# Kernel optimization log

Measured on AMD Instinct MI355X. Metric: run time of the kernel, lower is better.

Reference implementation:

```python
import jax, jax.numpy as jnp
import numpy as np
from jax import lax

TAU = 2.0        # LIF membrane time constant
EPS = 1e-5       # BatchNorm eps
ALPHA = 4.0      # surrogate sigmoid sharpness (spikingjelly default)
HEADS = 8
SCALE = 0.125

@jax.custom_vjp
def heaviside(x):
    return (x >= 0.0).astype(x.dtype)

def _h_fwd(x):
    return heaviside(x), x

def _h_bwd(x, g):
    s = jax.nn.sigmoid(ALPHA * x)
    return (g * ALPHA * s * (1.0 - s),)

heaviside.defvjp(_h_fwd, _h_bwd)

def lif(x, vth):
    # multi-step LIF over leading time axis; hard reset to 0, detach_reset=True
    def step(v, xt):
        v = v + (xt - v) / TAU
        s = heaviside(v - vth)
        v = v * (1.0 - lax.stop_gradient(s))
        return v, s
    _, spikes = lax.scan(step, jnp.zeros_like(x[0]), x)
    return spikes

def conv_bn(x, W, gamma, beta, b=None):
    # 1x1 Conv1d == channel GEMM; BN in training mode (batch stats over (TB, N))
    y = jnp.einsum('oc,tcn->ton', W, x)
    if b is not None:
        y = y + b[None, :, None]
    mu = y.mean(axis=(0, 2), keepdims=True)
    var = y.var(axis=(0, 2), keepdims=True)
    return gamma[None, :, None] * (y - mu) * lax.rsqrt(var + EPS) + beta[None, :, None]

def setup_inputs() -> dict:
    key = jax.random.key(0)
    ks = jax.random.split(key, 8)
    T, B, C, H, W = 4, 16, 512, 16, 16
    s = 1.0 / np.sqrt(C)
    return {
        'x': jax.random.normal(ks[0], (T, B, C, H, W), dtype=jnp.float32),
        'qW': jax.random.normal(ks[1], (C, C), dtype=jnp.float32) * s,
        'q_gamma': jnp.ones((C,), jnp.float32), 'q_beta': jnp.zeros((C,), jnp.float32),
        'kW': jax.random.normal(ks[2], (C, C), dtype=jnp.float32) * s,
        'k_gamma': jnp.ones((C,), jnp.float32), 'k_beta': jnp.zeros((C,), jnp.float32),
        'vW': jax.random.normal(ks[3], (C, C), dtype=jnp.float32) * s,
        'v_gamma': jnp.ones((C,), jnp.float32), 'v_beta': jnp.zeros((C,), jnp.float32),
        'projW': jax.random.normal(ks[4], (C, C), dtype=jnp.float32) * s,
        'proj_b': jnp.zeros((C,), jnp.float32),
        'proj_gamma': jnp.ones((C,), jnp.float32), 'proj_beta': jnp.zeros((C,), jnp.float32),
    }

def reference(x, qW, q_gamma, q_beta, kW, k_gamma, k_beta, vW, v_gamma, v_beta,
              projW, proj_b, proj_gamma, proj_beta):
    T, B, C, H, W = x.shape
    N = H * W
    d = C // HEADS
    xf = x.reshape(T * B, C, N)

    def branch(Wc, g, b):
        y = conv_bn(xf, Wc, g, b).reshape(T, B, C, N)
        s = lif(y, 1.0)                               # binary spikes [T,B,C,N]
        # -> [T,B,heads,N,d]
        return s.transpose(0, 1, 3, 2).reshape(T, B, N, HEADS, d).transpose(0, 1, 3, 2, 4)

    q = branch(qW, q_gamma, q_beta)
    k = branch(kW, k_gamma, k_beta)
    v = branch(vW, v_gamma, v_beta)

    kv = jnp.einsum('tbhnd,tbhne->tbhde', k, v)       # linear attention [d,d]
    a = jnp.einsum('tbhnd,tbhde->tbhne', q, kv) * SCALE
    a = a.transpose(0, 1, 2, 4, 3).reshape(T, B, C, N)
    a = lif(a, 0.5).reshape(T * B, C, N)              # attn_lif, vth=0.5

    out = conv_bn(a, projW, proj_gamma, proj_beta, proj_b).reshape(T, B, C, N)
    out = lif(out, 1.0)
    return out.reshape(T, B, C, W, H)
```

## Files before the change

### kernel.cpp

```cpp
#include <hip/hip_runtime.h>

#define T_ 4
#define B_ 16
#define C_ 512
#define N_ 256
#define TB_ 64

using u64 = unsigned long long;
typedef int v4i __attribute__((ext_vector_type(4)));


__device__ __forceinline__ void digitize6(float xf, double scale, int d[6]) {
  double m = (double)xf * scale;
  long long t = (long long)rint(m);
#pragma unroll
  for (int s = 5; s >= 0; --s) {
    int dig = (int)((t + 128) & 255) - 128;
    d[s] = dig;
    t = (t - dig) >> 8;
  }
}

__device__ __forceinline__ void digitize5(float xf, double scale, int d[5]) {
  double m = (double)xf * scale;
  long long t = (long long)rint(m);
#pragma unroll
  for (int s = 4; s >= 0; --s) {
    int dig = (int)((t + 128) & 255) - 128;
    d[s] = dig;
    t = (t - dig) >> 8;
  }
}

__device__ __forceinline__ void dig4(float xv, int d[4]) {
  float c = fminf(fmaxf(xv, -7.999999f), 7.999999f);
  int m = (int)rintf(c * 268435456.0f);
#pragma unroll
  for (int t = 3; t >= 0; --t) {
    int dd = ((m + 128) & 255) - 128;
    d[t] = dd;
    m = (m - dd) >> 8;
  }
}

__device__ __forceinline__ void gload16(const void* g, void* l) {
  __builtin_amdgcn_global_load_lds(
      (const __attribute__((address_space(1))) unsigned int*)(unsigned long long)g,
      (__attribute__((address_space(3))) unsigned int*)(unsigned long long)l,
      16, 0, 0);
}


__global__ __launch_bounds__(256) void predig_x(
    const float* __restrict__ X, char* __restrict__ Xd4)
{
  const int cb = blockIdx.x * 64;
  const int nb = blockIdx.y * 64;
  const int tb = blockIdx.z;
  const int n  = threadIdx.x & 63;
  const int c0 = (threadIdx.x >> 6) * 16;
  int dg[16][4];
#pragma unroll
  for (int j = 0; j < 16; ++j) {
    float xv = X[((size_t)tb * C_ + cb + c0 + j) * N_ + nb + n];
    dig4(xv, dg[j]);
  }
#pragma unroll
  for (int t = 0; t < 4; ++t) {
    unsigned w[4];
#pragma unroll
    for (int q = 0; q < 4; ++q)
      w[q] = (unsigned)(dg[4*q+0][t] & 255)
           | ((unsigned)(dg[4*q+1][t] & 255) << 8)
           | ((unsigned)(dg[4*q+2][t] & 255) << 16)
           | ((unsigned)(dg[4*q+3][t] & 255) << 24);
    uint4 u; u.x = w[0]; u.y = w[1]; u.z = w[2]; u.w = w[3];
    *reinterpret_cast<uint4*>(
        &Xd4[(((size_t)tb * N_ + nb + n) * 4 + t) * C_ + cb + c0]) = u;
  }
}

__global__ __launch_bounds__(128) void decomp_w5i(
    const float* __restrict__ W, char* __restrict__ Wsl)
{
  const int o = blockIdx.x;
  const int k4 = threadIdx.x * 4;
  float4 w4 = *reinterpret_cast<const float4*>(&W[(size_t)o * C_ + k4]);
  int d[4][5];
  digitize5(w4.x, 0x1p39, d[0]);
  digitize5(w4.y, 0x1p39, d[1]);
  digitize5(w4.z, 0x1p39, d[2]);
  digitize5(w4.w, 0x1p39, d[3]);
#pragma unroll
  for (int s = 0; s < 5; ++s) {
    unsigned u = (unsigned)(d[0][s] & 255) | ((unsigned)(d[1][s] & 255) << 8)
               | ((unsigned)(d[2][s] & 255) << 16) | ((unsigned)(d[3][s] & 255) << 24);
    *reinterpret_cast<unsigned*>(&Wsl[((size_t)o * 5 + s) * C_ + k4]) = u;
  }
}

template<int XP>
__global__ __launch_bounds__(256) void gemm_s(
    const char* __restrict__ Bp, const char* __restrict__ Wsl,
    double* __restrict__ Y)
{
  __shared__ v4i Als[2][5][64][4];
  __shared__ v4i Bls[2][XP][64][4];
  const int tb = blockIdx.z;
  const int ob = blockIdx.y * 64;
  const int nb = blockIdx.x * 64;
  const int tid = threadIdx.x;
  const int lane = tid & 63;
  const int wv = tid >> 6;
  const int wo = wv * 16;
  const int lr = lane & 15;
  const int lg = lane >> 4;

  v4i acc[5][4] = {};

  const int sow = wv * 16 + (lane >> 2);
  const int acs = (lane & 3) ^ ((sow >> 1) & 3);
  const char* asrc[5];
#pragma unroll
  for (int s = 0; s < 5; ++s)
    asrc[s] = Wsl + ((size_t)(ob + sow) * 5 + s) * C_ + acs * 16;

  const int s_slot = lane & 3;
  const char* bsrc[(XP == 4) ? 4 : 1];
  if (XP == 4) {
#pragma unroll
    for (int r = 0; r < 4; ++r) {
      int sn = r * 16 + (lane >> 2);
      bsrc[r] = Bp + (((size_t)tb * N_ + nb + sn) * 4 + wv) * C_
              + ((s_slot ^ ((sn >> 1) & 3)) * 16);
    }
  } else {
    int sn = wv * 16 + (lane >> 2);
    bsrc[0] = Bp + ((size_t)tb * N_ + nb + sn) * C_
            + ((s_slot ^ ((sn >> 1) & 3)) * 16);
  }

#define STAGE_(buf, cb) do {                                              \
    _Pragma("unroll")                                                     \
    for (int s_ = 0; s_ < 5; ++s_)                                        \
      gload16(asrc[s_] + (cb), &Als[buf][s_][wv * 16][0]);                \
    if (XP == 4) {                                                        \
      _Pragma("unroll")                                                   \
      for (int r_ = 0; r_ < 4; ++r_)                                      \
        gload16(bsrc[r_] + (cb), &Bls[buf][wv][r_ * 16][0]);              \
    } else {                                                              \
      gload16(bsrc[0] + (cb), &Bls[buf][0][wv * 16][0]);                  \
    }                                                                     \
  } while (0)

  STAGE_(0, 0);
  __syncthreads();

#pragma unroll
  for (int i = 0; i < 8; ++i) {
    const int cur = i & 1;
    const int cb = i * 64;
    if (i < 7) STAGE_(cur ^ 1, cb + 64);
    __builtin_amdgcn_sched_barrier(0);
    v4i Af[5];
#pragma unroll
    for (int s = 0; s < 5; ++s) {
      const int o = wo + lr;
      Af[s] = Als[cur][s][o][lg ^ ((o >> 1) & 3)];
    }
    v4i Bf[XP][4];
#pragma unroll
    for (int t = 0; t < XP; ++t)
#pragma unroll
      for (int nt = 0; nt < 4; ++nt) {
        const int n = nt * 16 + lr;
        Bf[t][nt] = Bls[cur][t][n][lg ^ ((n >> 1) & 3)];
      }
#pragma unroll
    for (int s = 0; s < 5; ++s)
#pragma unroll
      for (int t = 0; t < XP; ++t) {
        if (s + t <= 4) {
#pragma unroll
          for (int nt = 0; nt < 4; ++nt)
            acc[s + t][nt] = __builtin_amdgcn_mfma_i32_16x16x64_i8(
                Af[s], Bf[t][nt], acc[s + t][nt], 0, 0, 0);
        }
      }
    if (i < 7) __syncthreads();
  }
#undef STAGE_

  const double W0 = (XP == 4) ? 0x1p-11 : 0x1p-7;
#pragma unroll
  for (int nt = 0; nt < 4; ++nt)
#pragma unroll
    for (int r = 0; r < 4; ++r) {
      double y = 0.0;
      double wgt = W0;
#pragma unroll
      for (int u = 0; u < 5; ++u) {
        y = fma((double)acc[u][nt][r], wgt, y);
        wgt *= 0x1p-8;
      }
      int o = ob + wo + lg * 4 + r;
      int n = nb + nt * 16 + lr;
      Y[((size_t)tb * C_ + o) * N_ + n] = y;
    }
}

__global__ __launch_bounds__(256) void bn_stats_part(
    const double* __restrict__ Y, double* __restrict__ part)
{
  const int ch = blockIdx.x >> 3;
  const int g  = blockIdx.x & 7;
  const int n = threadIdx.x;
  double s = 0.0, s2 = 0.0;
#pragma unroll
  for (int k = 0; k < 8; ++k) {
    int tb = g * 8 + k;
    double v = Y[((size_t)tb * C_ + ch) * N_ + n];
    s += v;
    s2 = fma(v, v, s2);
  }
  __shared__ double rs[256], rq[256];
  rs[n] = s; rq[n] = s2;
  __syncthreads();
  for (int off = 128; off > 0; off >>= 1) {
    if (n < off) { rs[n] += rs[n + off]; rq[n] += rq[n + off]; }
    __syncthreads();
  }
  if (n == 0) {
    part[(size_t)(ch * 8 + g) * 2]     = rs[0];
    part[(size_t)(ch * 8 + g) * 2 + 1] = rq[0];
  }
}

__device__ __forceinline__ void stats_from_part(
    const double* __restrict__ part, int ch, double& mu, double& rsig)
{
  double s = 0.0, s2 = 0.0;
#pragma unroll
  for (int g = 0; g < 8; ++g) {
    s  += part[(size_t)(ch * 8 + g) * 2];
    s2 += part[(size_t)(ch * 8 + g) * 2 + 1];
  }
  mu = s * (1.0 / 16384.0);
  double var = s2 * (1.0 / 16384.0) - mu * mu;
  rsig = 1.0 / sqrt(var + 1e-5);
}

__global__ __launch_bounds__(256) void attn16(
    const u64* __restrict__ qb, const u64* __restrict__ kb,
    const u64* __restrict__ vb, short* __restrict__ A16)
{
  __shared__ u64 kw[64][4], vw[64][4], qw[64][4];
  __shared__ int kvs[64][64];
  const int h  = blockIdx.x & 7;
  const int tb = blockIdx.x >> 3;
  const int tid = threadIdx.x;
  {
    int dd = tid >> 2, w = tid & 3;
    size_t base = ((size_t)tb * C_ + h * 64 + dd) * 4 + w;
    kw[dd][w] = kb[base];
    vw[dd][w] = vb[base];
    qw[dd][w] = qb[base];
  }
  __syncthreads();
  {
    int dd = tid >> 2;
    int e0 = (tid & 3) << 4;
    u64 k0 = kw[dd][0], k1 = kw[dd][1], k2 = kw[dd][2], k3 = kw[dd][3];
    for (int e = e0; e < e0 + 16; ++e) {
      int c = __popcll(k0 & vw[e][0]) + __popcll(k1 & vw[e][1])
            + __popcll(k2 & vw[e][2]) + __popcll(k3 & vw[e][3]);
      kvs[dd][e] = c;
    }
  }
  __syncthreads();
  const int n = tid;
  u64 qmask = 0;
  {
    int wsel = n >> 6, sh = n & 63;
#pragma unroll
    for (int dd = 0; dd < 64; ++dd)
      qmask |= ((qw[dd][wsel] >> sh) & 1ull) << dd;
  }
  short* Ap = A16 + ((size_t)tb * C_ + h * 64) * N_ + n;
  for (int e = 0; e < 64; ++e) {
    int s = 0;
#pragma unroll
    for (int dd = 0; dd < 64; ++dd) {
      int m = -(int)((qmask >> dd) & 1ull);
      s += kvs[dd][e] & m;
    }
    Ap[(size_t)e * N_] = (short)s;
  }
}

__global__ __launch_bounds__(256) void attn_lif_sp(
    const short* __restrict__ A16, char* __restrict__ Sp8)
{
  const int nb = blockIdx.x * 64;
  const int cb = blockIdx.y * 64;
  const int b  = blockIdx.z;
  const int n  = threadIdx.x & 63;
  const int c0 = (threadIdx.x >> 6) * 16;
  unsigned char sp[4][16];
#pragma unroll
  for (int j = 0; j < 16; ++j) {
    int c = cb + c0 + j;
    float v = 0.f;
#pragma unroll
    for (int t = 0; t < T_; ++t) {
      float a = 0.125f * (float)A16[((size_t)(t * B_ + b) * C_ + c) * N_ + nb + n];
      v = (v + a) * 0.5f;
      bool s = (v >= 0.5f);
      sp[t][j] = s ? 1 : 0;
      if (s) v = 0.f;
    }
  }
#pragma unroll
  for (int t = 0; t < T_; ++t) {
    unsigned w[4];
#pragma unroll
    for (int q = 0; q < 4; ++q)
      w[q] = (unsigned)sp[t][4*q+0] | ((unsigned)sp[t][4*q+1] << 8)
           | ((unsigned)sp[t][4*q+2] << 16) | ((unsigned)sp[t][4*q+3] << 24);
    uint4 u; u.x = w[0]; u.y = w[1]; u.z = w[2]; u.w = w[3];
    *reinterpret_cast<uint4*>(
        &Sp8[((size_t)(t * B_ + b) * N_ + nb + n) * C_ + cb + c0]) = u;
  }
}

__global__ __launch_bounds__(256) void bn_lif_bits(
    const double* __restrict__ Y, const double* __restrict__ part,
    const float* __restrict__ gamma, const float* __restrict__ beta,
    double vth, u64* __restrict__ bits)
{
  const int o = blockIdx.x & (C_ - 1);
  const int b = blockIdx.x >> 9;
  const int n = threadIdx.x;
  double mu, rsig;
  stats_from_part(part, o, mu, rsig);
  const double g = (double)gamma[o], be = (double)beta[o];
  double v = 0.0;
#pragma unroll
  for (int t = 0; t < T_; ++t) {
    double y  = Y[((size_t)(t * B_ + b) * C_ + o) * N_ + n];
    double yn = (y - mu) * rsig * g + be;
    v = v + (yn - v) * 0.5;
    bool sp = (v >= vth);
    u64 m = __ballot(sp);
    if ((n & 63) == 0)
      bits[((size_t)(t * B_ + b) * C_ + o) * (N_ / 64) + (n >> 6)] = m;
    if (sp) v = 0.0;
  }
}

__global__ __launch_bounds__(256) void bn_lif_out(
    const double* __restrict__ Y, const double* __restrict__ part,
    const float* __restrict__ gamma, const float* __restrict__ beta,
    float* __restrict__ out)
{
  const int o = blockIdx.x & (C_ - 1);
  const int b = blockIdx.x >> 9;
  const int n = threadIdx.x;
  double mu, rsig;
  stats_from_part(part, o, mu, rsig);
  const double g = (double)gamma[o], be = (double)beta[o];
  double v = 0.0;
#pragma unroll
  for (int t = 0; t < T_; ++t) {
    double y  = Y[((size_t)(t * B_ + b) * C_ + o) * N_ + n];
    double yn = (y - mu) * rsig * g + be;
    v = v + (yn - v) * 0.5;
    bool sp = (v >= 1.0);
    out[((size_t)(t * B_ + b) * C_ + o) * N_ + n] = sp ? 1.0f : 0.0f;
    if (sp) v = 0.0;
  }
}


__global__ __launch_bounds__(128) void decomp_w(
    const float* __restrict__ W, char* __restrict__ Wsl)
{
  const int o = blockIdx.x;
  const int k4 = threadIdx.x * 4;
  float4 w4 = *reinterpret_cast<const float4*>(&W[(size_t)o * C_ + k4]);
  int d[4][6];
  digitize6(w4.x, 0x1p47, d[0]);
  digitize6(w4.y, 0x1p47, d[1]);
  digitize6(w4.z, 0x1p47, d[2]);
  digitize6(w4.w, 0x1p47, d[3]);
#pragma unroll
  for (int s = 0; s < 6; ++s) {
    unsigned u = (unsigned)(d[0][s] & 255) | ((unsigned)(d[1][s] & 255) << 8)
               | ((unsigned)(d[2][s] & 255) << 16) | ((unsigned)(d[3][s] & 255) << 24);
    *reinterpret_cast<unsigned*>(&Wsl[(size_t)s * C_ * C_ + (size_t)o * C_ + k4]) = u;
  }
}

template<int XS>
__global__ __launch_bounds__(256) void gemm_i8(
    const float* __restrict__ X, const char* __restrict__ Wsl,
    double* __restrict__ Y)
{
  __shared__ char Xs[XS][64][72];
  const int tb = blockIdx.z;
  const int ob = blockIdx.y * 64;
  const int nb = blockIdx.x * 64;
  const int tid = threadIdx.x;
  const int lane = tid & 63;
  const int wv = tid >> 6;
  const int wo = (wv & 1) * 32;
  const int wn = (wv >> 1) * 32;
  const int lr = lane & 15;
  const int lg = lane >> 4;

  constexpr int NU = (XS == 6) ? 7 : 6;
  v4i acc[NU][2][2] = {};

  const int sn = tid & 63;
  const int kq = (tid >> 6) * 4;

  for (int cb = 0; cb < C_; cb += 64) {
    __syncthreads();
#pragma unroll
    for (int st = 0; st < 4; ++st) {
      int k0 = kq + 16 * st;
      int dg[4][6];
#pragma unroll
      for (int j = 0; j < 4; ++j) {
        float xv = X[((size_t)tb * C_ + cb + k0 + j) * N_ + nb + sn];
        digitize6(xv, 0x1p43, dg[j]);
      }
#pragma unroll
      for (int t = 0; t < XS; ++t) {
        unsigned u = (unsigned)(dg[0][t] & 255) | ((unsigned)(dg[1][t] & 255) << 8)
                   | ((unsigned)(dg[2][t] & 255) << 16) | ((unsigned)(dg[3][t] & 255) << 24);
        *reinterpret_cast<unsigned*>(&Xs[t][sn][k0]) = u;
      }
    }
    __syncthreads();

    v4i Bf[XS][2];
#pragma unroll
    for (int t = 0; t < XS; ++t)
#pragma unroll
      for (int nt = 0; nt < 2; ++nt) {
        const char* p = &Xs[t][wn + nt * 16 + lr][lg * 16];
        int2 lo = *reinterpret_cast<const int2*>(p);
        int2 hi = *reinterpret_cast<const int2*>(p + 8);
        v4i b; b[0] = lo.x; b[1] = lo.y; b[2] = hi.x; b[3] = hi.y;
        Bf[t][nt] = b;
      }

#pragma unroll
    for (int s = 0; s < 6; ++s) {
      v4i Af[2];
#pragma unroll
      for (int ot = 0; ot < 2; ++ot) {
        const char* ap = Wsl + (size_t)s * C_ * C_
                       + (size_t)(ob + wo + ot * 16 + lr) * C_ + cb + lg * 16;
        Af[ot] = *reinterpret_cast<const v4i*>(ap);
      }
#pragma unroll
      for (int t = 0; t < XS; ++t) {
        if (s + t <= 6) {
#pragma unroll
          for (int ot = 0; ot < 2; ++ot)
#pragma unroll
            for (int nt = 0; nt < 2; ++nt)
              acc[s + t][ot][nt] = __builtin_amdgcn_mfma_i32_16x16x64_i8(
                  Af[ot], Bf[t][nt], acc[s + t][ot][nt], 0, 0, 0);
        }
      }
    }
  }

  const double WGT[7] = {0x1p-10, 0x1p-18, 0x1p-26, 0x1p-34,
                         0x1p-42, 0x1p-50, 0x1p-58};
#pragma unroll
  for (int ot = 0; ot < 2; ++ot)
#pragma unroll
    for (int nt = 0; nt < 2; ++nt)
#pragma unroll
      for (int r = 0; r < 4; ++r) {
        double y = 0.0;
#pragma unroll
        for (int u = 0; u < NU; ++u)
          y = fma((double)acc[u][ot][nt][r], WGT[u], y);
        int o = ob + wo + ot * 16 + lg * 4 + r;
        int n = nb + wn + nt * 16 + lr;
        Y[((size_t)tb * C_ + o) * N_ + n] = y;
      }
}

__global__ __launch_bounds__(256) void attn_kernel(
    const u64* __restrict__ qb, const u64* __restrict__ kb,
    const u64* __restrict__ vb, float* __restrict__ A)
{
  __shared__ u64 kw[64][4], vw[64][4], qw[64][4];
  __shared__ int kvs[64][64];
  const int h  = blockIdx.x & 7;
  const int tb = blockIdx.x >> 3;
  const int tid = threadIdx.x;
  {
    int dd = tid >> 2, w = tid & 3;
    size_t base = ((size_t)tb * C_ + h * 64 + dd) * 4 + w;
    kw[dd][w] = kb[base];
    vw[dd][w] = vb[base];
    qw[dd][w] = qb[base];
  }
  __syncthreads();
  {
    int dd = tid >> 2;
    int e0 = (tid & 3) << 4;
    u64 k0 = kw[dd][0], k1 = kw[dd][1], k2 = kw[dd][2], k3 = kw[dd][3];
    for (int e = e0; e < e0 + 16; ++e) {
      int c = __popcll(k0 & vw[e][0]) + __popcll(k1 & vw[e][1])
            + __popcll(k2 & vw[e][2]) + __popcll(k3 & vw[e][3]);
      kvs[dd][e] = c;
    }
  }
  __syncthreads();
  const int n = tid;
  u64 qmask = 0;
  {
    int wsel = n >> 6, sh = n & 63;
#pragma unroll
    for (int dd = 0; dd < 64; ++dd)
      qmask |= ((qw[dd][wsel] >> sh) & 1ull) << dd;
  }
  float* Ap = A + ((size_t)tb * C_ + h * 64) * N_ + n;
  for (int e = 0; e < 64; ++e) {
    int s = 0;
#pragma unroll
    for (int dd = 0; dd < 64; ++dd) {
      int m = -(int)((qmask >> dd) & 1ull);
      s += kvs[dd][e] & m;
    }
    Ap[(size_t)e * N_] = (float)s * 0.125f;
  }
}

__global__ __launch_bounds__(256) void attn_lif(float* __restrict__ A)
{
  const size_t i = (size_t)blockIdx.x * 256 + threadIdx.x;
  const size_t stride = (size_t)B_ * C_ * N_;
  float v = 0.f;
#pragma unroll
  for (int t = 0; t < T_; ++t) {
    float a = A[t * stride + i];
    v = v + (a - v) * 0.5f;
    bool sp = (v >= 0.5f);
    A[t * stride + i] = sp ? 1.0f : 0.0f;
    if (sp) v = 0.f;
  }
}

__global__ __launch_bounds__(256) void bn_stats(
    const double* __restrict__ Y, double* __restrict__ stats)
{
  const int o = blockIdx.x;
  const int n = threadIdx.x;
  double s = 0.0, s2 = 0.0;
  for (int tb = 0; tb < TB_; ++tb) {
    double v = Y[((size_t)tb * C_ + o) * N_ + n];
    s += v;
    s2 = fma(v, v, s2);
  }
  __shared__ double rs[256], rq[256];
  rs[n] = s; rq[n] = s2;
  __syncthreads();
  for (int off = 128; off > 0; off >>= 1) {
    if (n < off) { rs[n] += rs[n + off]; rq[n] += rq[n + off]; }
    __syncthreads();
  }
  if (n == 0) {
    double mu  = rs[0] * (1.0 / 16384.0);
    double var = rq[0] * (1.0 / 16384.0) - mu * mu;
    stats[o]      = mu;
    stats[C_ + o] = 1.0 / sqrt(var + 1e-5);
  }
}

__global__ __launch_bounds__(256) void bn_lif_bits_fb(
    const double* __restrict__ Y, const double* __restrict__ stats,
    const float* __restrict__ gamma, const float* __restrict__ beta,
    double vth, u64* __restrict__ bits)
{
  const int o = blockIdx.x & (C_ - 1);
  const int b = blockIdx.x >> 9;
  const int n = threadIdx.x;
  const double mu = stats[o], rsig = stats[C_ + o];
  const double g = (double)gamma[o], be = (double)beta[o];
  double v = 0.0;
#pragma unroll
  for (int t = 0; t < T_; ++t) {
    double y  = Y[((size_t)(t * B_ + b) * C_ + o) * N_ + n];
    double yn = (y - mu) * rsig * g + be;
    v = v + (yn - v) * 0.5;
    bool sp = (v >= vth);
    u64 m = __ballot(sp);
    if ((n & 63) == 0)
      bits[((size_t)(t * B_ + b) * C_ + o) * (N_ / 64) + (n >> 6)] = m;
    if (sp) v = 0.0;
  }
}

__global__ __launch_bounds__(256) void bn_lif_out_fb(
    const double* __restrict__ Y, const double* __restrict__ stats,
    const float* __restrict__ gamma, const float* __restrict__ beta,
    float* __restrict__ out)
{
  const int o = blockIdx.x & (C_ - 1);
  const int b = blockIdx.x >> 9;
  const int n = threadIdx.x;
  const double mu = stats[o], rsig = stats[C_ + o];
  const double g = (double)gamma[o], be = (double)beta[o];
  double v = 0.0;
#pragma unroll
  for (int t = 0; t < T_; ++t) {
    double y  = Y[((size_t)(t * B_ + b) * C_ + o) * N_ + n];
    double yn = (y - mu) * rsig * g + be;
    v = v + (yn - v) * 0.5;
    bool sp = (v >= 1.0);
    out[((size_t)(t * B_ + b) * C_ + o) * N_ + n] = sp ? 1.0f : 0.0f;
    if (sp) v = 0.0;
  }
}

extern "C" void kernel_launch(void* const* d_in, const int* in_sizes, int n_in,
                              void* d_out, int out_size, void* d_ws, size_t ws_size,
                              hipStream_t stream)
{
  const float* x    = (const float*)d_in[0];
  const float* qW   = (const float*)d_in[1];
  const float* qg   = (const float*)d_in[2];
  const float* qbt  = (const float*)d_in[3];
  const float* kW   = (const float*)d_in[4];
  const float* kg   = (const float*)d_in[5];
  const float* kbt  = (const float*)d_in[6];
  const float* vW   = (const float*)d_in[7];
  const float* vg   = (const float*)d_in[8];
  const float* vbt  = (const float*)d_in[9];
  const float* pW   = (const float*)d_in[10];
  const float* pg   = (const float*)d_in[12];
  const float* pbt  = (const float*)d_in[13];

  char* ws = (char*)d_ws;
  double* yD    = (double*)ws;
  u64*    bitsQ = (u64*)(ws + 100663296);
  u64*    bitsK = (u64*)(ws + 101711872);
  u64*    bitsV = (u64*)(ws + 102760448);
  double* stats = (double*)(ws + 103809024);

  if (ws_size >= 105390080ull) {
    char*   Xd4  = ws + 67108864;
    short*  A16  = (short*)(ws + 67108864);
    char*   Sp8  = ws + 67108864 + 16777216;
    char*   Wsl5 = ws + 103817216;
    double* part = (double*)(ws + 105127936);

    dim3 ggrid(4, 8, 64);

    predig_x<<<dim3(8, 4, 64), 256, 0, stream>>>(x, Xd4);
    decomp_w5i<<<512, 128, 0, stream>>>(qW, Wsl5);
    gemm_s<4><<<ggrid, 256, 0, stream>>>(Xd4, Wsl5, yD);
    bn_stats_part<<<4096, 256, 0, stream>>>(yD, part);
    bn_lif_bits<<<8192, 256, 0, stream>>>(yD, part, qg, qbt, 1.0, bitsQ);
    decomp_w5i<<<512, 128, 0, stream>>>(kW, Wsl5);
    gemm_s<4><<<ggrid, 256, 0, stream>>>(Xd4, Wsl5, yD);
    bn_stats_part<<<4096, 256, 0, stream>>>(yD, part);
    bn_lif_bits<<<8192, 256, 0, stream>>>(yD, part, kg, kbt, 1.0, bitsK);
    decomp_w5i<<<512, 128, 0, stream>>>(vW, Wsl5);
    gemm_s<4><<<ggrid, 256, 0, stream>>>(Xd4, Wsl5, yD);
    bn_stats_part<<<4096, 256, 0, stream>>>(yD, part);
    bn_lif_bits<<<8192, 256, 0, stream>>>(yD, part, vg, vbt, 1.0, bitsV);
    attn16<<<512, 256, 0, stream>>>(bitsQ, bitsK, bitsV, A16);
    attn_lif_sp<<<dim3(4, 8, 16), 256, 0, stream>>>(A16, Sp8);
    decomp_w5i<<<512, 128, 0, stream>>>(pW, Wsl5);
    gemm_s<1><<<ggrid, 256, 0, stream>>>(Sp8, Wsl5, yD);
    bn_stats_part<<<4096, 256, 0, stream>>>(yD, part);
    bn_lif_out<<<8192, 256, 0, stream>>>(yD, part, pg, pbt, (float*)d_out);
  } else {
    float* A    = (float*)(ws + 67108864);
    char*  WslA = ws + 67108864;
    char*  WslB = ws + 100663296;

    dim3 ggrid(4, 8, 64);

    decomp_w<<<512, 128, 0, stream>>>(qW, WslA);
    gemm_i8<6><<<ggrid, 256, 0, stream>>>(x, WslA, yD);
    bn_stats<<<512, 256, 0, stream>>>(yD, stats);
    bn_lif_bits_fb<<<8192, 256, 0, stream>>>(yD, stats, qg, qbt, 1.0, bitsQ);
    decomp_w<<<512, 128, 0, stream>>>(kW, WslA);
    gemm_i8<6><<<ggrid, 256, 0, stream>>>(x, WslA, yD);
    bn_stats<<<512, 256, 0, stream>>>(yD, stats);
    bn_lif_bits_fb<<<8192, 256, 0, stream>>>(yD, stats, kg, kbt, 1.0, bitsK);
    decomp_w<<<512, 128, 0, stream>>>(vW, WslA);
    gemm_i8<6><<<ggrid, 256, 0, stream>>>(x, WslA, yD);
    bn_stats<<<512, 256, 0, stream>>>(yD, stats);
    bn_lif_bits_fb<<<8192, 256, 0, stream>>>(yD, stats, vg, vbt, 1.0, bitsV);
    attn_kernel<<<512, 256, 0, stream>>>(bitsQ, bitsK, bitsV, A);
    attn_lif<<<8192, 256, 0, stream>>>(A);
    decomp_w<<<512, 128, 0, stream>>>(pW, WslB);
    gemm_i8<1><<<ggrid, 256, 0, stream>>>(A, WslB, yD);
    bn_stats<<<512, 256, 0, stream>>>(yD, stats);
    bn_lif_out_fb<<<8192, 256, 0, stream>>>(yD, stats, pg, pbt, (float*)d_out);
  }
}
```

Baseline: 408.1 us.

## Fuse BN statistics into GEMM epilogue via fixed-point integer atomics

```diff
diff --git a/kernel.cpp b/kernel.cpp
--- a/kernel.cpp
+++ b/kernel.cpp
@@ -102,7 +102,7 @@
 template<int XP>
 __global__ __launch_bounds__(256) void gemm_s(
     const char* __restrict__ Bp, const char* __restrict__ Wsl,
-    double* __restrict__ Y)
+    double* __restrict__ Y, u64* __restrict__ istats)
 {
   __shared__ v4i Als[2][5][64][4];
   __shared__ v4i Bls[2][XP][64][4];
@@ -192,6 +192,7 @@
 #undef STAGE_
 
   const double W0 = (XP == 4) ? 0x1p-11 : 0x1p-7;
+  double ys[4][4];
 #pragma unroll
   for (int nt = 0; nt < 4; ++nt)
 #pragma unroll
@@ -203,51 +204,27 @@
         y = fma((double)acc[u][nt][r], wgt, y);
         wgt *= 0x1p-8;
       }
+      ys[nt][r] = y;
       int o = ob + wo + lg * 4 + r;
       int n = nb + nt * 16 + lr;
       Y[((size_t)tb * C_ + o) * N_ + n] = y;
     }
-}
-
-__global__ __launch_bounds__(256) void bn_stats_part(
-    const double* __restrict__ Y, double* __restrict__ part)
-{
-  const int ch = blockIdx.x >> 3;
-  const int g  = blockIdx.x & 7;
-  const int n = threadIdx.x;
-  double s = 0.0, s2 = 0.0;
-#pragma unroll
-  for (int k = 0; k < 8; ++k) {
-    int tb = g * 8 + k;
-    double v = Y[((size_t)tb * C_ + ch) * N_ + n];
-    s += v;
-    s2 = fma(v, v, s2);
-  }
-  __shared__ double rs[256], rq[256];
-  rs[n] = s; rq[n] = s2;
-  __syncthreads();
-  for (int off = 128; off > 0; off >>= 1) {
-    if (n < off) { rs[n] += rs[n + off]; rq[n] += rq[n + off]; }
-    __syncthreads();
-  }
-  if (n == 0) {
-    part[(size_t)(ch * 8 + g) * 2]     = rs[0];
-    part[(size_t)(ch * 8 + g) * 2 + 1] = rq[0];
-  }
-}
-
-__device__ __forceinline__ void stats_from_part(
-    const double* __restrict__ part, int ch, double& mu, double& rsig)
-{
-  double s = 0.0, s2 = 0.0;
-#pragma unroll
-  for (int g = 0; g < 8; ++g) {
-    s  += part[(size_t)(ch * 8 + g) * 2];
-    s2 += part[(size_t)(ch * 8 + g) * 2 + 1];
-  }
-  mu = s * (1.0 / 16384.0);
-  double var = s2 * (1.0 / 16384.0) - mu * mu;
-  rsig = 1.0 / sqrt(var + 1e-5);
+#pragma unroll
+  for (int r = 0; r < 4; ++r) {
+    double s = ys[0][r] + ys[1][r] + ys[2][r] + ys[3][r];
+    double q = ys[0][r] * ys[0][r] + ys[1][r] * ys[1][r]
+             + ys[2][r] * ys[2][r] + ys[3][r] * ys[3][r];
+#pragma unroll
+    for (int m = 1; m < 16; m <<= 1) {
+      s += __shfl_xor(s, m, 64);
+      q += __shfl_xor(q, m, 64);
+    }
+    if (lr == 0) {
+      int o = ob + wo + lg * 4 + r;
+      atomicAdd(&istats[o],      (u64)(long long)llrint(s * 0x1p40));
+      atomicAdd(&istats[C_ + o], (u64)llrint(q * 0x1p35));
+    }
+  }
 }
 
 __global__ __launch_bounds__(256) void attn16(
@@ -334,15 +311,16 @@
 }
 
 __global__ __launch_bounds__(256) void bn_lif_bits(
-    const double* __restrict__ Y, const double* __restrict__ part,
+    const double* __restrict__ Y, const u64* __restrict__ istats,
     const float* __restrict__ gamma, const float* __restrict__ beta,
     double vth, u64* __restrict__ bits)
 {
   const int o = blockIdx.x & (C_ - 1);
   const int b = blockIdx.x >> 9;
   const int n = threadIdx.x;
-  double mu, rsig;
-  stats_from_part(part, o, mu, rsig);
+  const double mu  = (double)(long long)istats[o] * 0x1p-54;
+  const double ex2 = (double)istats[C_ + o] * 0x1p-49;
+  const double rsig = 1.0 / sqrt(ex2 - mu * mu + 1e-5);
   const double g = (double)gamma[o], be = (double)beta[o];
   double v = 0.0;
 #pragma unroll
@@ -359,15 +337,16 @@
 }
 
 __global__ __launch_bounds__(256) void bn_lif_out(
-    const double* __restrict__ Y, const double* __restrict__ part,
+    const double* __restrict__ Y, const u64* __restrict__ istats,
     const float* __restrict__ gamma, const float* __restrict__ beta,
     float* __restrict__ out)
 {
   const int o = blockIdx.x & (C_ - 1);
   const int b = blockIdx.x >> 9;
   const int n = threadIdx.x;
-  double mu, rsig;
-  stats_from_part(part, o, mu, rsig);
+  const double mu  = (double)(long long)istats[o] * 0x1p-54;
+  const double ex2 = (double)istats[C_ + o] * 0x1p-49;
+  const double rsig = 1.0 / sqrt(ex2 - mu * mu + 1e-5);
   const double g = (double)gamma[o], be = (double)beta[o];
   double v = 0.0;
 #pragma unroll
@@ -655,40 +634,40 @@
   u64*    bitsQ = (u64*)(ws + 100663296);
   u64*    bitsK = (u64*)(ws + 101711872);
   u64*    bitsV = (u64*)(ws + 102760448);
-  double* stats = (double*)(ws + 103809024);
+  u64*    istat = (u64*)(ws + 103809024);
 
   if (ws_size >= 105390080ull) {
-    char*   Xd4  = ws + 67108864;
-    short*  A16  = (short*)(ws + 67108864);
-    char*   Sp8  = ws + 67108864 + 16777216;
-    char*   Wsl5 = ws + 103817216;
-    double* part = (double*)(ws + 105127936);
+    char*  Xd4  = ws + 67108864;
+    short* A16  = (short*)(ws + 67108864);
+    char*  Sp8  = ws + 67108864 + 16777216;
+    char*  Wsl5 = ws + 103817216;
 
     dim3 ggrid(4, 8, 64);
 
     predig_x<<<dim3(8, 4, 64), 256, 0, stream>>>(x, Xd4);
     decomp_w5i<<<512, 128, 0, stream>>>(qW, Wsl5);
-    gemm_s<4><<<ggrid, 256, 0, stream>>>(Xd4, Wsl5, yD);
-    bn_stats_part<<<4096, 256, 0, stream>>>(yD, part);
-    bn_lif_bits<<<8192, 256, 0, stream>>>(yD, part, qg, qbt, 1.0, bitsQ);
+    hipMemsetAsync(istat, 0, 8192, stream);
+    gemm_s<4><<<ggrid, 256, 0, stream>>>(Xd4, Wsl5, yD, istat);
+    bn_lif_bits<<<8192, 256, 0, stream>>>(yD, istat, qg, qbt, 1.0, bitsQ);
     decomp_w5i<<<512, 128, 0, stream>>>(kW, Wsl5);
-    gemm_s<4><<<ggrid, 256, 0, stream>>>(Xd4, Wsl5, yD);
-    bn_stats_part<<<4096, 256, 0, stream>>>(yD, part);
-    bn_lif_bits<<<8192, 256, 0, stream>>>(yD, part, kg, kbt, 1.0, bitsK);
+    hipMemsetAsync(istat, 0, 8192, stream);
+    gemm_s<4><<<ggrid, 256, 0, stream>>>(Xd4, Wsl5, yD, istat);
+    bn_lif_bits<<<8192, 256, 0, stream>>>(yD, istat, kg, kbt, 1.0, bitsK);
     decomp_w5i<<<512, 128, 0, stream>>>(vW, Wsl5);
-    gemm_s<4><<<ggrid, 256, 0, stream>>>(Xd4, Wsl5, yD);
-    bn_stats_part<<<4096, 256, 0, stream>>>(yD, part);
-    bn_lif_bits<<<8192, 256, 0, stream>>>(yD, part, vg, vbt, 1.0, bitsV);
+    hipMemsetAsync(istat, 0, 8192, stream);
+    gemm_s<4><<<ggrid, 256, 0, stream>>>(Xd4, Wsl5, yD, istat);
+    bn_lif_bits<<<8192, 256, 0, stream>>>(yD, istat, vg, vbt, 1.0, bitsV);
     attn16<<<512, 256, 0, stream>>>(bitsQ, bitsK, bitsV, A16);
     attn_lif_sp<<<dim3(4, 8, 16), 256, 0, stream>>>(A16, Sp8);
     decomp_w5i<<<512, 128, 0, stream>>>(pW, Wsl5);
-    gemm_s<1><<<ggrid, 256, 0, stream>>>(Sp8, Wsl5, yD);
-    bn_stats_part<<<4096, 256, 0, stream>>>(yD, part);
-    bn_lif_out<<<8192, 256, 0, stream>>>(yD, part, pg, pbt, (float*)d_out);
+    hipMemsetAsync(istat, 0, 8192, stream);
+    gemm_s<1><<<ggrid, 256, 0, stream>>>(Sp8, Wsl5, yD, istat);
+    bn_lif_out<<<8192, 256, 0, stream>>>(yD, istat, pg, pbt, (float*)d_out);
   } else {
-    float* A    = (float*)(ws + 67108864);
-    char*  WslA = ws + 67108864;
-    char*  WslB = ws + 100663296;
+    float*  A     = (float*)(ws + 67108864);
+    char*   WslA  = ws + 67108864;
+    char*   WslB  = ws + 100663296;
+    double* stats = (double*)(ws + 103809024);
 
     dim3 ggrid(4, 8, 64);
 
```

After: 396.2 us. 1.03x faster.
